# Kernel optimization log

Hardware: AMD Instinct MI355X
Metric: run time of the kernel (lower is better)

## Reference

```python
import jax, jax.numpy as jnp
import numpy as np

D_MODEL = 2048
HEADS = 16
INNER = 8192
SEQ = 2048
BATCH = 1  # source code's mask.reshape(B,1,L,L) requires B==1
EPS = 1e-5


def _layer_norm(x, gamma, beta):
    mu = jnp.mean(x, axis=-1, keepdims=True)
    var = jnp.mean(jnp.square(x - mu), axis=-1, keepdims=True)
    return (x - mu) * jax.lax.rsqrt(var + EPS) * gamma + beta


def setup_inputs() -> dict:
    key = jax.random.key(0)
    ks = jax.random.split(key, 14)
    s = 0.02
    return {
        "x": jax.random.normal(ks[0], (BATCH, SEQ, D_MODEL), jnp.float32),
        # weights stored as (in, out)
        "Wqkv": jax.random.normal(ks[1], (D_MODEL, 3 * D_MODEL), jnp.float32) * s,
        "bqkv": jnp.zeros((3 * D_MODEL,), jnp.float32),
        "Wo": jax.random.normal(ks[2], (D_MODEL, D_MODEL), jnp.float32) * s,
        "bo": jnp.zeros((D_MODEL,), jnp.float32),
        "W1": jax.random.normal(ks[3], (D_MODEL, INNER), jnp.float32) * s,
        "b1": jnp.zeros((INNER,), jnp.float32),
        "W2": jax.random.normal(ks[4], (INNER, D_MODEL), jnp.float32) * s,
        "b2": jnp.zeros((D_MODEL,), jnp.float32),
        "g1": jnp.ones((D_MODEL,), jnp.float32),
        "be1": jnp.zeros((D_MODEL,), jnp.float32),
        "g2": jnp.ones((D_MODEL,), jnp.float32),
        "be2": jnp.zeros((D_MODEL,), jnp.float32),
    }


def reference(x, Wqkv, bqkv, Wo, bo, W1, b1, W2, b2, g1, be1, g2, be2):
    B, L, D = x.shape
    H, hd = HEADS, D // HEADS
    qkv = x @ Wqkv + bqkv                       # [B,L,3D]
    q, k, v = jnp.split(qkv, 3, axis=-1)
    q = q.reshape(B, L, H, hd)
    k = k.reshape(B, L, H, hd)
    v = v.reshape(B, L, H, hd)
    # NOTE: faithful to source, scale is 1/sqrt(D) not 1/sqrt(head_dim)
    scores = jnp.einsum("bqhd,bkhd->bhqk", q, k) / jnp.sqrt(jnp.float32(D))
    causal = jnp.tril(jnp.ones((L, L), bool))   # [L,L] broadcast over B,H
    scores = jnp.where(causal, scores, -jnp.inf)
    attn = jax.nn.softmax(scores, axis=-1)      # dropout = identity (eval)
    out = jnp.einsum("bhqk,bkhd->bqhd", attn, v).reshape(B, L, D)
    lin = out @ Wo + bo
    h = _layer_norm(x + lin, g1, be1)
    ff = jax.nn.gelu(h @ W1 + b1, approximate=False) @ W2 + b2
    return _layer_norm(h + ff, g2, be2)
```

## Files before the change

### kernel.cpp

```cpp
#include <hip/hip_runtime.h>
#include <hip/hip_bf16.h>

typedef unsigned short u16;
typedef __attribute__((ext_vector_type(8))) short frag8;
typedef __attribute__((ext_vector_type(4))) float facc4;

#define L_SEQ 2048
#define D_MODEL 2048
#define N_HEADS 16
#define HEAD_D 128
#define N_QKV 6144
#define D_INNER 8192

__device__ __forceinline__ u16 f2b(float f) {
    __hip_bfloat16 h = __float2bfloat16(f);
    return *reinterpret_cast<u16*>(&h);
}

__device__ __forceinline__ float b2f(u16 u) {
    __hip_bfloat16 h = *reinterpret_cast<__hip_bfloat16*>(&u);
    return __bfloat162float(h);
}

__device__ __forceinline__ void gload_lds16(const void* g, void* l) {
    __builtin_amdgcn_global_load_lds(
        (const __attribute__((address_space(1))) unsigned int*)g,
        (__attribute__((address_space(3))) unsigned int*)l, 16, 0, 0);
}

__device__ __forceinline__ float gelu_exact(float x) {
    return 0.5f * x * (1.0f + erff(x * 0.7071067811865475f));
}

__global__ void cvt_bf16_kernel(const float* __restrict__ in, u16* __restrict__ out, int n) {
    int i = blockIdx.x * blockDim.x + threadIdx.x;
    int stride = gridDim.x * blockDim.x;
    for (; i < n; i += stride) out[i] = f2b(in[i]);
}

__global__ void tr_cvt_kernel(const float* __restrict__ in, u16* __restrict__ out, int R, int C) {
    __shared__ float t[32][33];
    int bx = blockIdx.x * 32;
    int by = blockIdx.y * 32;
    int tx = threadIdx.x, ty = threadIdx.y;
#pragma unroll
    for (int k = 0; k < 32; k += 8) t[ty + k][tx] = in[(size_t)(by + ty + k) * C + bx + tx];
    __syncthreads();
#pragma unroll
    for (int k = 0; k < 32; k += 8) out[(size_t)(bx + ty + k) * R + by + tx] = f2b(t[tx][ty + k]);
}

__global__ __launch_bounds__(256) void gemm_bt(const u16* __restrict__ A, const u16* __restrict__ Bt,
                                               const float* __restrict__ bias, float* __restrict__ Cout,
                                               int M, int N, int K) {
    __shared__ u16 lA[128 * 64];
    __shared__ u16 lB[128 * 64];
    const int tid = threadIdx.x;
    const int lane = tid & 63, wid = tid >> 6;
    const int wr = wid >> 1, wc = wid & 1;
    const int l15 = lane & 15, g4 = lane >> 4;
    const int bm = blockIdx.y, bn = blockIdx.x;

    const int arow = tid >> 3;
    const int acol = (tid & 7) * 8;
    const size_t abase = (size_t)(bm * 128) * K + acol;
    const size_t bbase = (size_t)(bn * 128) * K + acol;

    facc4 acc[4][4] = {};

    for (int k0 = 0; k0 < K; k0 += 64) {
        if (k0) __syncthreads();
#pragma unroll
        for (int i = 0; i < 4; i++) {
            gload_lds16(A + abase + (size_t)(i * 32 + arow) * K + k0, &lA[i * 2048 + tid * 8]);
            gload_lds16(Bt + bbase + (size_t)(i * 32 + arow) * K + k0, &lB[i * 2048 + tid * 8]);
        }
        __syncthreads();
#pragma unroll
        for (int kk = 0; kk < 64; kk += 32) {
            frag8 af[4], bf[4];
#pragma unroll
            for (int m = 0; m < 4; m++)
                af[m] = *(const frag8*)&lA[(wr * 64 + m * 16 + l15) * 64 + kk + g4 * 8];
#pragma unroll
            for (int n = 0; n < 4; n++)
                bf[n] = *(const frag8*)&lB[(wc * 64 + n * 16 + l15) * 64 + kk + g4 * 8];
#pragma unroll
            for (int m = 0; m < 4; m++)
#pragma unroll
                for (int n = 0; n < 4; n++)
                    acc[m][n] = __builtin_amdgcn_mfma_f32_16x16x32_bf16(af[m], bf[n], acc[m][n], 0, 0, 0);
        }
    }

    const int row0 = bm * 128 + wr * 64 + g4 * 4;
    const int col0 = bn * 128 + wc * 64 + l15;
#pragma unroll
    for (int n = 0; n < 4; n++) {
        const int col = col0 + n * 16;
        const float bv = bias[col];
#pragma unroll
        for (int m = 0; m < 4; m++)
#pragma unroll
            for (int r = 0; r < 4; r++)
                Cout[(size_t)(row0 + m * 16 + r) * N + col] = acc[m][n][r] + bv;
    }
}

template <int EPI>
__global__ __launch_bounds__(512, 2) void gemm256(const u16* __restrict__ A, const u16* __restrict__ Bt,
                                                  const float* __restrict__ bias, void* __restrict__ Cout,
                                                  float* __restrict__ q0, float* __restrict__ q1,
                                                  float* __restrict__ q2, float* __restrict__ q3,
                                                  int M, int N, int K, int kseg, int nbn) {
    __shared__ u16 lds[4 * 16384];
    const int tid = threadIdx.x;
    const int lane = tid & 63, wid = tid >> 6;
    const int wm = wid >> 2, wn = wid & 3;
    const int l15 = lane & 15, g4 = lane >> 4;

    const int nwg = gridDim.x;
    const int q8 = nwg >> 3;
    const int wg = (blockIdx.x & 7) * q8 + (blockIdx.x >> 3);
    const int bn = wg % nbn, bm = wg / nbn;
    const int kb = blockIdx.z * kseg;
    const int ksz = (blockIdx.z == (int)gridDim.z - 1) ? (K - kb) : kseg;
    const int nt = ksz >> 5;

    const int rA = tid >> 2;
    const int swzT = ((tid >> 3) & 3) << 4;
    const int srcE = ((((tid & 3) << 4) ^ swzT) >> 1);
    const u16* Ab = A + (size_t)(bm * 256 + rA) * K + kb + srcE;
    const u16* Bb = Bt + (size_t)(bn * 256 + rA) * K + kb + srcE;
    const size_t rstride = (size_t)128 * K;

    int aoff[8], boff[4];
#pragma unroll
    for (int mf = 0; mf < 8; mf++) {
        const int rowl = wm * 128 + mf * 16 + l15;
        aoff[mf] = rowl * 32 + (((g4 * 16) ^ (((rowl >> 1) & 3) << 4)) >> 1);
    }
#pragma unroll
    for (int nf = 0; nf < 4; nf++) {
        const int rowl = wn * 64 + nf * 16 + l15;
        boff[nf] = rowl * 32 + (((g4 * 16) ^ (((rowl >> 1) & 3) << 4)) >> 1);
    }

    auto stageA = [&](int tt) {
        u16* sA = &lds[(tt & 3) * 16384];
        const u16* g = Ab + (size_t)tt * 32;
        gload_lds16(g, sA + tid * 8);
        gload_lds16(g + rstride, sA + 4096 + tid * 8);
    };
    auto stageB = [&](int tt) {
        u16* sB = &lds[(tt & 3) * 16384 + 8192];
        const u16* g = Bb + (size_t)tt * 32;
        gload_lds16(g, sB + tid * 8);
        gload_lds16(g + rstride, sB + 4096 + tid * 8);
    };

    facc4 acc[8][4] = {};

    stageA(0); stageB(0);
    stageA(1); stageB(1);
    stageA(2); stageB(2);
    asm volatile("s_waitcnt vmcnt(8)" ::: "memory");
    __builtin_amdgcn_s_barrier();
    __builtin_amdgcn_sched_barrier(0);

    for (int t = 0; t < nt; ++t) {
        const u16* sA = &lds[(t & 3) * 16384];
        const u16* sB = sA + 8192;
        frag8 b0[4], ap[2];
#pragma unroll
        for (int i = 0; i < 4; i++) b0[i] = *(const frag8*)&sB[boff[i]];
        ap[0] = *(const frag8*)&sA[aoff[0]];
        ap[1] = *(const frag8*)&sA[aoff[1]];
        if (t + 3 < nt) stageA(t + 3);
        __builtin_amdgcn_s_setprio(1);
#pragma unroll
        for (int m = 0; m < 2; m++)
#pragma unroll
            for (int nf = 0; nf < 4; nf++)
                acc[m][nf] = __builtin_amdgcn_mfma_f32_16x16x32_bf16(ap[m], b0[nf], acc[m][nf], 0, 0, 0);
        __builtin_amdgcn_s_setprio(0);
        ap[0] = *(const frag8*)&sA[aoff[2]];
        ap[1] = *(const frag8*)&sA[aoff[3]];
        __builtin_amdgcn_s_setprio(1);
#pragma unroll
        for (int m = 0; m < 2; m++)
#pragma unroll
            for (int nf = 0; nf < 4; nf++)
                acc[2 + m][nf] = __builtin_amdgcn_mfma_f32_16x16x32_bf16(ap[m], b0[nf], acc[2 + m][nf], 0, 0, 0);
        __builtin_amdgcn_s_setprio(0);
        __builtin_amdgcn_s_barrier();
        ap[0] = *(const frag8*)&sA[aoff[4]];
        ap[1] = *(const frag8*)&sA[aoff[5]];
        if (t + 3 < nt) stageB(t + 3);
        __builtin_amdgcn_s_setprio(1);
#pragma unroll
        for (int m = 0; m < 2; m++)
#pragma unroll
            for (int nf = 0; nf < 4; nf++)
                acc[4 + m][nf] = __builtin_amdgcn_mfma_f32_16x16x32_bf16(ap[m], b0[nf], acc[4 + m][nf], 0, 0, 0);
        __builtin_amdgcn_s_setprio(0);
        ap[0] = *(const frag8*)&sA[aoff[6]];
        ap[1] = *(const frag8*)&sA[aoff[7]];
        __builtin_amdgcn_s_setprio(1);
#pragma unroll
        for (int m = 0; m < 2; m++)
#pragma unroll
            for (int nf = 0; nf < 4; nf++)
                acc[6 + m][nf] = __builtin_amdgcn_mfma_f32_16x16x32_bf16(ap[m], b0[nf], acc[6 + m][nf], 0, 0, 0);
        __builtin_amdgcn_s_setprio(0);
        if (t + 3 < nt)
            asm volatile("s_waitcnt vmcnt(8)" ::: "memory");
        else if (t + 2 < nt)
            asm volatile("s_waitcnt vmcnt(4)" ::: "memory");
        else
            asm volatile("s_waitcnt vmcnt(0)" ::: "memory");
        __builtin_amdgcn_s_barrier();
        __builtin_amdgcn_sched_barrier(0);
    }

    const int row0 = bm * 256 + wm * 128 + g4 * 4;
    const int col0 = bn * 256 + wn * 64 + l15;
    float* fout;
    if (EPI == 3) {
        const int z = blockIdx.z;
        fout = (z == 0) ? q0 : (z == 1) ? q1 : (z == 2) ? q2 : q3;
    } else {
        fout = (float*)Cout;
    }
#pragma unroll
    for (int nf = 0; nf < 4; nf++) {
        const int col = col0 + nf * 16;
        const float bv = (EPI == 3) ? 0.0f : bias[col];
#pragma unroll
        for (int mf = 0; mf < 8; mf++) {
#pragma unroll
            for (int r = 0; r < 4; r++) {
                const int row = row0 + mf * 16 + r;
                float v = acc[mf][nf][r] + bv;
                if (EPI == 2) v = gelu_exact(v);
                if (EPI == 0 || EPI == 3)
                    fout[(size_t)row * N + col] = v;
                else
                    ((u16*)Cout)[(size_t)row * N + col] = f2b(v);
            }
        }
    }
}

__global__ __launch_bounds__(256) void attn_kernel(const u16* __restrict__ qkv, u16* __restrict__ out) {
    __shared__ u16 kT[64 * 128];
    __shared__ u16 vT[128 * 64];
    const int h = blockIdx.y;
    const int qb = (blockIdx.y < 8) ? ((int)gridDim.x - 1 - (int)blockIdx.x) : (int)blockIdx.x;
    const int tid = threadIdx.x;
    const int lane = tid & 63, w = tid >> 6;
    const int l15 = lane & 15, g4 = lane >> 4;
    const int q0 = qb * 64 + w * 16;
    const float scale = 0.022097086912079608f;

    frag8 qf[4];
    {
        const u16* qrow = qkv + (size_t)(q0 + l15) * N_QKV + h * HEAD_D + g4 * 8;
#pragma unroll
        for (int c = 0; c < 4; c++) qf[c] = *(const frag8*)(qrow + c * 32);
    }

    float m_run = -1e30f, l_run = 0.0f;
    facc4 o[8] = {};

    const int src0 = ((g4 & 1) << 5) + l15;
    const int src1 = src0 + 16;
    const bool hi = (g4 & 2) != 0;

    const int nt = qb + 1;
    for (int t = 0; t < nt; ++t) {
        const int kbase = t * 64;
        if (t) __syncthreads();
        const u16* kg_ptr = qkv + (size_t)kbase * N_QKV + D_MODEL + h * HEAD_D;
        const u16* vg_ptr = kg_ptr + D_MODEL;
        uint4 vv[4];
#pragma unroll
        for (int i = 0; i < 4; ++i)
            vv[i] = *(const uint4*)(vg_ptr + (size_t)lane * N_QKV + w * 32 + i * 8);
#pragma unroll
        for (int p = 0; p < 4; ++p) {
            const int c = p * 256 + tid;
            const int row = c >> 4;
            const int colb = (c & 15) << 4;
            const int srcb = colb ^ ((row & 7) << 4);
            gload_lds16(kg_ptr + (size_t)row * N_QKV + (srcb >> 1), &kT[c * 8]);
        }
#pragma unroll
        for (int i = 0; i < 4; ++i) {
            const u16* pv = (const u16*)&vv[i];
#pragma unroll
            for (int e = 0; e < 8; ++e) {
                const int d = w * 32 + i * 8 + e;
                vT[d * 64 + ((((lane >> 3) ^ (d & 7)) << 3) | (lane & 7))] = pv[e];
            }
        }
        __syncthreads();

        const bool last = (t == nt - 1);

        float st[16];
        float mx = -1e30f;
#pragma unroll
        for (int ks = 0; ks < 4; ++ks) {
            const bool active = !last || (ks <= w);
            if (active) {
                facc4 s = {};
                const int kl = ks * 16 + l15;
#pragma unroll
                for (int c = 0; c < 4; ++c) {
                    const int colb = (g4 * 16 + c * 64) ^ ((kl & 7) << 4);
                    frag8 kf = *(const frag8*)&kT[kl * 128 + (colb >> 1)];
                    s = __builtin_amdgcn_mfma_f32_16x16x32_bf16(kf, qf[c], s, 0, 0, 0);
                }
#pragma unroll
                for (int r = 0; r < 4; ++r) {
                    float v = s[r] * scale;
                    if (last) {
                        const int key = kbase + ks * 16 + g4 * 4 + r;
                        if (key > q0 + l15) v = -1e30f;
                    }
                    st[ks * 4 + r] = v;
                    mx = fmaxf(mx, v);
                }
            } else {
#pragma unroll
                for (int r = 0; r < 4; ++r) st[ks * 4 + r] = -1e30f;
            }
        }

        mx = fmaxf(mx, __shfl_xor(mx, 16));
        mx = fmaxf(mx, __shfl_xor(mx, 32));
        const bool skip = __all(mx <= m_run + 8.0f);
        const float m_new = skip ? m_run : fmaxf(m_run, mx);
        const float alpha = __expf(m_run - m_new);
        float ps = 0.0f;
        uint2 pb[4];
#pragma unroll
        for (int ks = 0; ks < 4; ++ks) {
            const float p0 = __expf(st[ks * 4 + 0] - m_new);
            const float p1 = __expf(st[ks * 4 + 1] - m_new);
            const float p2 = __expf(st[ks * 4 + 2] - m_new);
            const float p3 = __expf(st[ks * 4 + 3] - m_new);
            ps += (p0 + p1) + (p2 + p3);
            pb[ks].x = (unsigned)f2b(p0) | ((unsigned)f2b(p1) << 16);
            pb[ks].y = (unsigned)f2b(p2) | ((unsigned)f2b(p3) << 16);
        }
        ps += __shfl_xor(ps, 16);
        ps += __shfl_xor(ps, 32);
        l_run = l_run * alpha + ps;
        m_run = m_new;
        if (!skip) {
#pragma unroll
            for (int c8 = 0; c8 < 8; ++c8)
#pragma unroll
                for (int r = 0; r < 4; ++r) o[c8][r] *= alpha;
        }

#pragma unroll
        for (int kp = 0; kp < 2; ++kp) {
            const bool kp_active = !last || (kp == 0) || (w >= 2);
            if (kp_active) {
                const uint2 a = pb[2 * kp], b = pb[2 * kp + 1];
                const unsigned a0 = __shfl(a.x, src0), a1 = __shfl(a.y, src0);
                const unsigned a2 = __shfl(a.x, src1), a3 = __shfl(a.y, src1);
                const unsigned b0 = __shfl(b.x, src0), b1 = __shfl(b.y, src0);
                const unsigned b2 = __shfl(b.x, src1), b3 = __shfl(b.y, src1);
                union { unsigned u[4]; frag8 f; } pu;
                pu.u[0] = hi ? b0 : a0;
                pu.u[1] = hi ? b1 : a1;
                pu.u[2] = hi ? b2 : a2;
                pu.u[3] = hi ? b3 : a3;
                const frag8 pf = pu.f;
#pragma unroll
                for (int c8 = 0; c8 < 8; ++c8) {
                    const int d = c8 * 16 + l15;
                    const int ch = (((kp * 4 + g4) ^ (l15 & 7)) << 3);
                    frag8 vf = *(const frag8*)&vT[d * 64 + ch];
                    o[c8] = __builtin_amdgcn_mfma_f32_16x16x32_bf16(vf, pf, o[c8], 0, 0, 0);
                }
            }
        }
    }

    const float inv_l = 1.0f / l_run;
    u16* orow = out + (size_t)(q0 + l15) * D_MODEL + h * HEAD_D;
#pragma unroll
    for (int c8 = 0; c8 < 8; ++c8) {
        uint2 st2;
        st2.x = (unsigned)f2b(o[c8][0] * inv_l) | ((unsigned)f2b(o[c8][1] * inv_l) << 16);
        st2.y = (unsigned)f2b(o[c8][2] * inv_l) | ((unsigned)f2b(o[c8][3] * inv_l) << 16);
        *(uint2*)&orow[c8 * 16 + g4 * 4] = st2;
    }
}

__global__ __launch_bounds__(256) void ln_kernel(const float* __restrict__ a, const float* __restrict__ b,
                                                 const float* __restrict__ gamma, const float* __restrict__ beta,
                                                 u16* __restrict__ outb) {
    __shared__ float red[8];
    const int row = blockIdx.x;
    const int tid = threadIdx.x;
    const float* pa = a + (size_t)row * D_MODEL;
    const float* pb = b + (size_t)row * D_MODEL;
    float v[8];
    float s = 0.0f, s2 = 0.0f;
#pragma unroll
    for (int i = 0; i < 8; i++) {
        const int c = tid + i * 256;
        const float x = pa[c] + pb[c];
        v[i] = x;
        s += x;
        s2 += x * x;
    }
#pragma unroll
    for (int off = 32; off; off >>= 1) {
        s += __shfl_xor(s, off);
        s2 += __shfl_xor(s2, off);
    }
    if ((tid & 63) == 0) { red[(tid >> 6) * 2] = s; red[(tid >> 6) * 2 + 1] = s2; }
    __syncthreads();
    s = red[0] + red[2] + red[4] + red[6];
    s2 = red[1] + red[3] + red[5] + red[7];
    const float mean = s * (1.0f / D_MODEL);
    const float var = s2 * (1.0f / D_MODEL) - mean * mean;
    const float rstd = rsqrtf(var + 1e-5f);
#pragma unroll
    for (int i = 0; i < 8; i++) {
        const int c = tid + i * 256;
        outb[(size_t)row * D_MODEL + c] = f2b((v[i] - mean) * rstd * gamma[c] + beta[c]);
    }
}

__global__ __launch_bounds__(256) void ln_part_kernel(const u16* __restrict__ hb,
                                                      const float* __restrict__ p0, const float* __restrict__ p1,
                                                      const float* __restrict__ p2, const float* __restrict__ p3,
                                                      int np, const float* __restrict__ bias,
                                                      const float* __restrict__ gamma, const float* __restrict__ beta,
                                                      float* __restrict__ outf) {
    __shared__ float red[8];
    const int row = blockIdx.x;
    const int tid = threadIdx.x;
    const size_t rb = (size_t)row * D_MODEL;
    float v[8];
    float s = 0.0f, s2 = 0.0f;
#pragma unroll
    for (int i = 0; i < 8; i++) {
        const int c = tid + i * 256;
        float x = b2f(hb[rb + c]) + bias[c] + p0[rb + c] + p1[rb + c];
        if (np > 2) x += p2[rb + c];
        if (np > 3) x += p3[rb + c];
        v[i] = x;
        s += x;
        s2 += x * x;
    }
#pragma unroll
    for (int off = 32; off; off >>= 1) {
        s += __shfl_xor(s, off);
        s2 += __shfl_xor(s2, off);
    }
    if ((tid & 63) == 0) { red[(tid >> 6) * 2] = s; red[(tid >> 6) * 2 + 1] = s2; }
    __syncthreads();
    s = red[0] + red[2] + red[4] + red[6];
    s2 = red[1] + red[3] + red[5] + red[7];
    const float mean = s * (1.0f / D_MODEL);
    const float var = s2 * (1.0f / D_MODEL) - mean * mean;
    const float rstd = rsqrtf(var + 1e-5f);
#pragma unroll
    for (int i = 0; i < 8; i++) {
        const int c = tid + i * 256;
        outf[rb + c] = (v[i] - mean) * rstd * gamma[c] + beta[c];
    }
}

extern "C" void kernel_launch(void* const* d_in, const int* in_sizes, int n_in,
                              void* d_out, int out_size, void* d_ws, size_t ws_size,
                              hipStream_t stream) {
    const float* x    = (const float*)d_in[0];
    const float* Wqkv = (const float*)d_in[1];
    const float* bqkv = (const float*)d_in[2];
    const float* Wo   = (const float*)d_in[3];
    const float* bo   = (const float*)d_in[4];
    const float* W1   = (const float*)d_in[5];
    const float* b1   = (const float*)d_in[6];
    const float* W2   = (const float*)d_in[7];
    const float* b2   = (const float*)d_in[8];
    const float* g1   = (const float*)d_in[9];
    const float* be1  = (const float*)d_in[10];
    const float* g2   = (const float*)d_in[11];
    const float* be2  = (const float*)d_in[12];

    char* ws = (char*)d_ws;
    const size_t MB = 1024 * 1024;
    u16*  xb     = (u16*)(ws + 0);
    u16*  WqkvT  = (u16*)(ws + 8 * MB);
    u16*  qkv    = (u16*)(ws + 32 * MB);
    u16*  attn_o = (u16*)(ws + 56 * MB);
    u16*  WoT    = (u16*)(ws + 8 * MB);
    float* proj  = (float*)(ws + 16 * MB);
    u16*  hb     = (u16*)(ws + 0);
    u16*  W1T    = (u16*)(ws + 8 * MB);
    u16*  f1     = (u16*)(ws + 40 * MB);
    u16*  W2T    = (u16*)(ws + 72 * MB);
    float* part0 = (float*)(ws + 8 * MB);
    float* part1 = (float*)(ws + 24 * MB);
    float* part2 = (float*)(ws + 104 * MB);
    float* part3 = (float*)(ws + 120 * MB);

    const int np = (ws_size >= 136 * MB) ? 4 : 3;
    const int kseg = (np == 4) ? 2048 : 2688;

    const dim3 b32(32, 8);

    cvt_bf16_kernel<<<2048, 256, 0, stream>>>(x, xb, L_SEQ * D_MODEL);
    tr_cvt_kernel<<<dim3(N_QKV / 32, D_MODEL / 32), b32, 0, stream>>>(Wqkv, WqkvT, D_MODEL, N_QKV);
    gemm256<1><<<dim3(192, 1, 1), 512, 0, stream>>>(xb, WqkvT, bqkv, qkv, nullptr, nullptr, nullptr, nullptr,
                                                    L_SEQ, N_QKV, D_MODEL, D_MODEL, 24);
    attn_kernel<<<dim3(L_SEQ / 64, N_HEADS), 256, 0, stream>>>(qkv, attn_o);
    tr_cvt_kernel<<<dim3(D_MODEL / 32, D_MODEL / 32), b32, 0, stream>>>(Wo, WoT, D_MODEL, D_MODEL);
    gemm_bt<<<dim3(D_MODEL / 128, L_SEQ / 128), 256, 0, stream>>>(attn_o, WoT, bo, proj, L_SEQ, D_MODEL, D_MODEL);
    ln_kernel<<<L_SEQ, 256, 0, stream>>>(x, proj, g1, be1, hb);
    tr_cvt_kernel<<<dim3(D_INNER / 32, D_MODEL / 32), b32, 0, stream>>>(W1, W1T, D_MODEL, D_INNER);
    gemm256<2><<<dim3(256, 1, 1), 512, 0, stream>>>(hb, W1T, b1, f1, nullptr, nullptr, nullptr, nullptr,
                                                    L_SEQ, D_INNER, D_MODEL, D_MODEL, 32);
    tr_cvt_kernel<<<dim3(D_MODEL / 32, D_INNER / 32), b32, 0, stream>>>(W2, W2T, D_INNER, D_MODEL);
    gemm256<3><<<dim3(64, 1, np), 512, 0, stream>>>(f1, W2T, nullptr, nullptr, part0, part1, part2, part3,
                                                    L_SEQ, D_MODEL, D_INNER, kseg, 8);
    ln_part_kernel<<<L_SEQ, 256, 0, stream>>>(hb, part0, part1, part2, part3, np, b2, g2, be2, (float*)d_out);
}
```

Measured before the change: 474.3 us.

## Vectorize conversion kernels, widen transpose tiles, and reorder GEMM tile mapping

The fp32-to-bf16 conversion now handles eight elements per thread with 128-bit loads and stores. The transpose-convert kernel uses 64x64 tiles with float4 reads and 16-byte bf16 writes, replacing the 32x32 tiled version with scalar accesses. The GEMM workgroup-to-tile mapping now walks M fastest instead of N, so neighbouring workgroups share the same weight columns, which may change L2 reuse. The conversion kernels are memory-bound, so wider accesses aim to cut their bandwidth overhead. For the W2 GEMM, nbm=8 equals the number of M tiles, so its mapping also changes.

```diff
diff --git a/kernel.cpp b/kernel.cpp
--- a/kernel.cpp
+++ b/kernel.cpp
@@ -32,22 +32,41 @@
     return 0.5f * x * (1.0f + erff(x * 0.7071067811865475f));
 }
 
-__global__ void cvt_bf16_kernel(const float* __restrict__ in, u16* __restrict__ out, int n) {
-    int i = blockIdx.x * blockDim.x + threadIdx.x;
-    int stride = gridDim.x * blockDim.x;
-    for (; i < n; i += stride) out[i] = f2b(in[i]);
-}
-
-__global__ void tr_cvt_kernel(const float* __restrict__ in, u16* __restrict__ out, int R, int C) {
-    __shared__ float t[32][33];
-    int bx = blockIdx.x * 32;
-    int by = blockIdx.y * 32;
-    int tx = threadIdx.x, ty = threadIdx.y;
-#pragma unroll
-    for (int k = 0; k < 32; k += 8) t[ty + k][tx] = in[(size_t)(by + ty + k) * C + bx + tx];
+__global__ __launch_bounds__(256) void cvt_bf16_kernel(const float* __restrict__ in, u16* __restrict__ out, int n) {
+    const int i = (blockIdx.x * 256 + threadIdx.x) * 8;
+    if (i >= n) return;
+    float4 a = *(const float4*)(in + i);
+    float4 b = *(const float4*)(in + i + 4);
+    u16 tmp[8];
+    tmp[0] = f2b(a.x); tmp[1] = f2b(a.y); tmp[2] = f2b(a.z); tmp[3] = f2b(a.w);
+    tmp[4] = f2b(b.x); tmp[5] = f2b(b.y); tmp[6] = f2b(b.z); tmp[7] = f2b(b.w);
+    *(uint4*)(out + i) = *(uint4*)tmp;
+}
+
+__global__ __launch_bounds__(256) void tr_cvt64(const float* __restrict__ in, u16* __restrict__ out, int R, int C) {
+    __shared__ float t[64][68];
+    const int bx = blockIdx.x * 64;
+    const int by = blockIdx.y * 64;
+    const int tid = threadIdx.x;
+    {
+        const int r = tid >> 2;
+        const int c4 = (tid & 3) * 16;
+        const float* src = in + (size_t)(by + r) * C + bx + c4;
+#pragma unroll
+        for (int j = 0; j < 4; ++j)
+            *(float4*)&t[r][c4 + 4 * j] = *(const float4*)(src + 4 * j);
+    }
     __syncthreads();
-#pragma unroll
-    for (int k = 0; k < 32; k += 8) out[(size_t)(bx + ty + k) * R + by + tx] = f2b(t[tx][ty + k]);
+    {
+        const int cc = tid >> 2;
+        const int rr0 = (tid & 3) * 16;
+        u16 tmp[16];
+#pragma unroll
+        for (int j = 0; j < 16; ++j) tmp[j] = f2b(t[rr0 + j][cc]);
+        u16* dst = out + (size_t)(bx + cc) * R + by + rr0;
+        *(uint4*)(dst) = *(uint4*)&tmp[0];
+        *(uint4*)(dst + 8) = *(uint4*)&tmp[8];
+    }
 }
 
 __global__ __launch_bounds__(256) void gemm_bt(const u16* __restrict__ A, const u16* __restrict__ Bt,
@@ -112,7 +131,7 @@
                                                   const float* __restrict__ bias, void* __restrict__ Cout,
                                                   float* __restrict__ q0, float* __restrict__ q1,
                                                   float* __restrict__ q2, float* __restrict__ q3,
-                                                  int M, int N, int K, int kseg, int nbn) {
+                                                  int M, int N, int K, int kseg, int nbm) {
     __shared__ u16 lds[4 * 16384];
     const int tid = threadIdx.x;
     const int lane = tid & 63, wid = tid >> 6;
@@ -122,7 +141,7 @@
     const int nwg = gridDim.x;
     const int q8 = nwg >> 3;
     const int wg = (blockIdx.x & 7) * q8 + (blockIdx.x >> 3);
-    const int bn = wg % nbn, bm = wg / nbn;
+    const int bm = wg % nbm, bn = wg / nbm;
     const int kb = blockIdx.z * kseg;
     const int ksz = (blockIdx.z == (int)gridDim.z - 1) ? (K - kb) : kseg;
     const int nt = ksz >> 5;
@@ -518,20 +537,18 @@
     const int np = (ws_size >= 136 * MB) ? 4 : 3;
     const int kseg = (np == 4) ? 2048 : 2688;
 
-    const dim3 b32(32, 8);
-
     cvt_bf16_kernel<<<2048, 256, 0, stream>>>(x, xb, L_SEQ * D_MODEL);
-    tr_cvt_kernel<<<dim3(N_QKV / 32, D_MODEL / 32), b32, 0, stream>>>(Wqkv, WqkvT, D_MODEL, N_QKV);
+    tr_cvt64<<<dim3(N_QKV / 64, D_MODEL / 64), 256, 0, stream>>>(Wqkv, WqkvT, D_MODEL, N_QKV);
     gemm256<1><<<dim3(192, 1, 1), 512, 0, stream>>>(xb, WqkvT, bqkv, qkv, nullptr, nullptr, nullptr, nullptr,
-                                                    L_SEQ, N_QKV, D_MODEL, D_MODEL, 24);
+                                                    L_SEQ, N_QKV, D_MODEL, D_MODEL, 8);
     attn_kernel<<<dim3(L_SEQ / 64, N_HEADS), 256, 0, stream>>>(qkv, attn_o);
-    tr_cvt_kernel<<<dim3(D_MODEL / 32, D_MODEL / 32), b32, 0, stream>>>(Wo, WoT, D_MODEL, D_MODEL);
+    tr_cvt64<<<dim3(D_MODEL / 64, D_MODEL / 64), 256, 0, stream>>>(Wo, WoT, D_MODEL, D_MODEL);
     gemm_bt<<<dim3(D_MODEL / 128, L_SEQ / 128), 256, 0, stream>>>(attn_o, WoT, bo, proj, L_SEQ, D_MODEL, D_MODEL);
     ln_kernel<<<L_SEQ, 256, 0, stream>>>(x, proj, g1, be1, hb);
-    tr_cvt_kernel<<<dim3(D_INNER / 32, D_MODEL / 32), b32, 0, stream>>>(W1, W1T, D_MODEL, D_INNER);
+    tr_cvt64<<<dim3(D_INNER / 64, D_MODEL / 64), 256, 0, stream>>>(W1, W1T, D_MODEL, D_INNER);
     gemm256<2><<<dim3(256, 1, 1), 512, 0, stream>>>(hb, W1T, b1, f1, nullptr, nullptr, nullptr, nullptr,
-                                                    L_SEQ, D_INNER, D_MODEL, D_MODEL, 32);
-    tr_cvt_kernel<<<dim3(D_MODEL / 32, D_INNER / 32), b32, 0, stream>>>(W2, W2T, D_INNER, D_MODEL);
+                                                    L_SEQ, D_INNER, D_MODEL, D_MODEL, 8);
+    tr_cvt64<<<dim3(D_MODEL / 64, D_INNER / 64), 256, 0, stream>>>(W2, W2T, D_INNER, D_MODEL);
     gemm256<3><<<dim3(64, 1, np), 512, 0, stream>>>(f1, W2T, nullptr, nullptr, part0, part1, part2, part3,
                                                     L_SEQ, D_MODEL, D_INNER, kseg, 8);
     ln_part_kernel<<<L_SEQ, 256, 0, stream>>>(hb, part0, part1, part2, part3, np, b2, g2, be2, (float*)d_out);
```

Result: no change. 472.2 us (-0.4%).
